# Kernel tuning notes

Hardware: AMD Instinct MI355X
Metric: run time of the kernel (lower is better)

Reference implementation:

```python
import jax, jax.numpy as jnp
import numpy as np

B, S, DM, H, NM, PRED = 32, 512, 512, 8, 4, 96
DK = DM // H
C1 = (NM + 7) // 2  # 5
C2 = (NM + 7) // 4  # 2
FC_IN = C2 * (S // 2)  # 512
EPS_NORM = 1e-12
EPS_LN = 1e-5


def _pos_encoding(seq_len, d):
    pos = np.arange(seq_len, dtype=np.float32)[:, None]
    div = np.exp(np.arange(0, d, 2, dtype=np.float32) * (-np.log(10000.0) / d))
    pe = np.zeros((seq_len, d), np.float32)
    pe[:, 0::2] = np.sin(pos * div)
    pe[:, 1::2] = np.cos(pos * div)
    return jnp.asarray(pe)

PE = _pos_encoding(S, DM)


def setup_inputs() -> dict:
    key = jax.random.key(0)
    ks = jax.random.split(key, 24)
    g = lambda k, shape, s: (jax.random.normal(k, shape, dtype=jnp.float32) * s)
    inp = {
        "x": g(ks[0], (B, S, 7), 1.0),
        "emb_W": g(ks[1], (4, DM), 0.5),
        "emb_b": jnp.zeros((DM,), jnp.float32),
        "Wq": g(ks[2], (NM, DM, DM), DM ** -0.5),
        "bq": jnp.zeros((NM, DM), jnp.float32),
        "Wk": g(ks[3], (NM, DM, DM), DM ** -0.5),
        "bk": jnp.zeros((NM, DM), jnp.float32),
        "Wv": g(ks[4], (NM, DM, DM), DM ** -0.5),
        "bv": jnp.zeros((NM, DM), jnp.float32),
        "Wo": g(ks[5], (NM, DM, DM), DM ** -0.5),
        "bo": jnp.zeros((NM, DM), jnp.float32),
        "conv1_w": g(ks[6], (C1, NM * DM, 3), (NM * DM * 3) ** -0.5),
        "conv1_b": jnp.zeros((C1,), jnp.float32),
        "conv2_w": g(ks[7], (C2, C1, 3), (C1 * 3) ** -0.5),
        "conv2_b": jnp.zeros((C2,), jnp.float32),
        "fc1_w": g(ks[8], (FC_IN, 256), FC_IN ** -0.5),
        "fc1_b": jnp.zeros((256,), jnp.float32),
        "fc2_w": g(ks[9], (256, 128), 256 ** -0.5),
        "fc2_b": jnp.zeros((128,), jnp.float32),
        "fc3_w": g(ks[10], (128, PRED), 128 ** -0.5),
        "fc3_b": jnp.zeros((PRED,), jnp.float32),
        "ln_g": jnp.ones((PRED,), jnp.float32),
        "ln_b": jnp.zeros((PRED,), jnp.float32),
    }
    return inp


def _l2norm(v):
    n = jnp.linalg.norm(v, axis=-1, keepdims=True)
    return v / jnp.maximum(n, EPS_NORM)


def reference(x, emb_W, emb_b, Wq, bq, Wk, bk, Wv, bv, Wo, bo,
              conv1_w, conv1_b, conv2_w, conv2_b,
              fc1_w, fc1_b, fc2_w, fc2_b, fc3_w, fc3_b, ln_g, ln_b):
    b, s, _ = x.shape
    static = x[:, :, :3]                     # [B,S,3]
    dynamic = x[:, :, 3:]                    # [B,S,4]
    # per-modality input: [dynamic_i | static] -> [B,M,S,4]
    mod_in = jnp.concatenate([
        dynamic.transpose(0, 2, 1)[..., None],
        jnp.broadcast_to(static[:, None], (b, NM, s, 3)),
    ], axis=-1)
    h = jnp.einsum('bmsf,fd->bmsd', mod_in, emb_W) + emb_b  # shared embedding
    h = h + PE[None, None, :s, :]

    # per-modality multi-head cosine attention (stacked over modality axis m)
    def proj(W, bias):
        y = jnp.einsum('bmsd,mde->bmse', h, W) + bias[None, :, None, :]
        return y.reshape(b, NM, s, H, DK).transpose(0, 1, 3, 2, 4)  # [B,M,H,S,DK]

    Q = _l2norm(proj(Wq, bq))
    K = _l2norm(proj(Wk, bk))
    V = proj(Wv, bv)
    scores = jnp.einsum('bmhsk,bmhtk->bmhst', Q, K)
    attn = jax.nn.softmax(scores, axis=-1)
    ctx = jnp.einsum('bmhst,bmhtk->bmhsk', attn, V)
    ctx = ctx.transpose(0, 1, 3, 2, 4).reshape(b, NM, s, DM)
    out = jnp.einsum('bmsd,mde->bmse', ctx, Wo) + bo[None, :, None, :]

    # concat modalities along feature dim: [B,S,M*DM]
    combined = out.transpose(0, 2, 1, 3).reshape(b, s, NM * DM)

    # conv stack (NCW layout), kernel 3, padding 1
    c = combined.transpose(0, 2, 1)  # [B, M*DM, S]
    dn = ('NCH', 'OIH', 'NCH')
    c = jax.lax.conv_general_dilated(c, conv1_w, (1,), ((1, 1),), dimension_numbers=dn) + conv1_b[None, :, None]
    c = jax.nn.elu(c)
    c = jax.lax.conv_general_dilated(c, conv2_w, (1,), ((1, 1),), dimension_numbers=dn) + conv2_b[None, :, None]
    c = jax.nn.elu(c)
    # max pool k=2 stride=2
    c = c.reshape(b, C2, s // 2, 2).max(axis=-1)
    flat = c.reshape(b, -1)  # [B, FC_IN]

    z = jax.nn.elu(flat @ fc1_w + fc1_b)
    z = jax.nn.elu(z @ fc2_w + fc2_b)
    z = z @ fc3_w + fc3_b  # [B, PRED]

    mu = jnp.mean(z, axis=-1, keepdims=True)
    var = jnp.var(z, axis=-1, keepdims=True)
    z = (z - mu) / jnp.sqrt(var + EPS_LN) * ln_g + ln_b
    return z.reshape(b, PRED, 1)
```

## Files before the change

### kernel.cpp

```cpp
#include <hip/hip_runtime.h>
#include <math.h>

typedef unsigned short u16;
typedef unsigned int u32;
typedef __attribute__((ext_vector_type(8))) short short8;
typedef __attribute__((ext_vector_type(4))) float f32x4;
typedef __attribute__((ext_vector_type(16))) float f32x16;
typedef __attribute__((ext_vector_type(4))) u32 u32x4;
typedef __attribute__((ext_vector_type(2))) u32 u32x2;

__device__ inline u16 f2b(float f) {
  u32 u = __builtin_bit_cast(u32, f);
  u32 r = u + 0x7fffu + ((u >> 16) & 1u);
  return (u16)(r >> 16);
}
__device__ inline float b2f(u16 b) {
  return __builtin_bit_cast(float, (u32)b << 16);
}
__device__ inline u32 cvtpk(float lo, float hi) {
  u32 r;
  asm("v_cvt_pk_bf16_f32 %0, %1, %2" : "=v"(r) : "v"(lo), "v"(hi));
  return r;
}
__device__ inline float eluf(float x) { return x > 0.f ? x : expf(x) - 1.f; }

__device__ inline f32x4 mfma16(short8 a, short8 b, f32x4 c) {
  return __builtin_amdgcn_mfma_f32_16x16x32_bf16(a, b, c, 0, 0, 0);
}
__device__ inline f32x16 mfma32(short8 a, short8 b, f32x16 c) {
  return __builtin_amdgcn_mfma_f32_32x32x16_bf16(a, b, c, 0, 0, 0);
}
__device__ inline void gload16(const u16* g, u16* l) {
  __builtin_amdgcn_global_load_lds((__attribute__((address_space(1))) void*)(g),
                                   (__attribute__((address_space(3))) void*)(l),
                                   16, 0, 0);
}

__global__ __launch_bounds__(256) void prep_misc(
    const float* __restrict__ emb_b, const float* __restrict__ bq,
    const float* __restrict__ bk, const float* __restrict__ bv,
    const float* __restrict__ Wq, const float* __restrict__ Wk,
    const float* __restrict__ Wv, const float* __restrict__ embW,
    const float* __restrict__ Wo, const float* __restrict__ bo,
    const float* __restrict__ w1, u16* __restrict__ A_pe,
    float* __restrict__ pb_bias, float* __restrict__ EW,
    u16* __restrict__ WEFFT, float* __restrict__ bias_t,
    u16* __restrict__ WTqkv) {
  __shared__ float smem[64 * 65];
  const int bid = blockIdx.x, t = threadIdx.x;
  if (bid < 512) {
    int s = bid;
    float div = __expf((2.f * t) * (-9.210340371976184f / 512.f));
    float arg = (float)s * div;
    A_pe[s * 512 + 2 * t] = f2b(__sinf(arg) + emb_b[2 * t]);
    A_pe[s * 512 + 2 * t + 1] = f2b(__cosf(arg) + emb_b[2 * t + 1]);
  } else if (bid < 536) {
    int i = (bid - 512) * 256 + t;
    int z = i >> 9, e = i & 511;
    int ty = z >> 2, m = z & 3;
    const float* bp = (ty == 0) ? bq : (ty == 1) ? bk : bv;
    pb_bias[i] = bp[m * 512 + e];
  } else if (bid < 584) {
    int idx = bid - 536;
    int z = idx >> 2, ch = idx & 3;
    const float* W =
        ((z < 4) ? Wq : (z < 8) ? Wk : Wv) + (long)(z & 3) * 262144;
    int el = t & 127, dh = t >> 7;
    int e = ch * 128 + el;
    float a[4] = {};
    for (int d = dh * 256; d < dh * 256 + 256; ++d) {
      float wv = W[(long)d * 512 + e];
#pragma unroll
      for (int f = 0; f < 4; ++f) a[f] += embW[f * 512 + d] * wv;
    }
#pragma unroll
    for (int f = 0; f < 4; ++f) smem[(dh * 4 + f) * 128 + el] = a[f];
    __syncthreads();
    if (t < 128) {
#pragma unroll
      for (int f = 0; f < 4; ++f)
        EW[((long)z * 4 + f) * 512 + e] =
            smem[f * 128 + el] + smem[(4 + f) * 128 + el];
    }
  } else if (bid < 1097) {
    const int wb = bid - 584;
    const int w = t >> 6, l = t & 63;
    if (wb < 512) {
      int idx = wb * 4 + w;
      int m = idx >> 9, d = idx & 511;
      const float* wrow = Wo + ((long)m * 512 + d) * 512;
      float a[15] = {};
#pragma unroll
      for (int i = 0; i < 8; ++i) {
        int e = l * 8 + i;
        float wv = wrow[e];
#pragma unroll
        for (int o = 0; o < 5; ++o)
#pragma unroll
          for (int k = 0; k < 3; ++k)
            a[o * 3 + k] += wv * w1[((long)o * 2048 + m * 512 + e) * 3 + k];
      }
#pragma unroll
      for (int j = 0; j < 15; ++j) {
        float v = a[j];
        for (int o = 1; o < 64; o <<= 1) v += __shfl_xor(v, o);
        if (l == 0) WEFFT[((long)m * 16 + j) * 512 + d] = f2b(v);
      }
      if (l == 0) WEFFT[((long)m * 16 + 15) * 512 + d] = 0;
    } else if (w == 0) {
      float a[15] = {};
      for (int c = l; c < 2048; c += 64) {
        float bv = bo[c];
#pragma unroll
        for (int o = 0; o < 5; ++o)
#pragma unroll
          for (int k = 0; k < 3; ++k)
            a[o * 3 + k] += bv * w1[((long)o * 2048 + c) * 3 + k];
      }
#pragma unroll
      for (int j = 0; j < 15; ++j) {
        float v = a[j];
        for (int o = 1; o < 64; o <<= 1) v += __shfl_xor(v, o);
        if (l == 0) bias_t[j] = v;
      }
      if (l == 0) bias_t[15] = 0.f;
    }
  } else {
    int bidt = bid - 1097;
    int mid = bidt >> 6, rest = bidt & 63;
    int d0 = (rest >> 3) * 64, e0 = (rest & 7) * 64;
    const float* W =
        ((mid < 4) ? Wq : (mid < 8) ? Wk : Wv) + (long)(mid & 3) * 262144;
    u16* WT = WTqkv + (long)mid * 262144;
    float(*tile)[65] = (float(*)[65])smem;
    int dr = t >> 2, ec = (t & 3) * 16;
#pragma unroll
    for (int j = 0; j < 16; j += 4) {
      float4 v = *(const float4*)&W[(long)(d0 + dr) * 512 + e0 + ec + j];
      tile[dr][ec + j] = v.x;
      tile[dr][ec + j + 1] = v.y;
      tile[dr][ec + j + 2] = v.z;
      tile[dr][ec + j + 3] = v.w;
    }
    __syncthreads();
    int er = t >> 2, dc = (t & 3) * 16;
    u16 tmp[16] __attribute__((aligned(16)));
#pragma unroll
    for (int j = 0; j < 16; ++j) tmp[j] = f2b(tile[dc + j][er]);
    *(short8*)&WT[(long)(e0 + er) * 512 + d0 + dc] = *(short8*)&tmp[0];
    *(short8*)&WT[(long)(e0 + er) * 512 + d0 + dc + 8] = *(short8*)&tmp[8];
  }
}

template <bool OBF>
__global__ __launch_bounds__(256) void gemm_bt(
    const u16* __restrict__ A, long sAz, int lda, const u16* __restrict__ BT,
    const float* __restrict__ bias, void* __restrict__ out, long sOz, int ldo) {
  __shared__ u16 As[3][128 * 32];
  __shared__ u16 Bs[3][128 * 32];
  const int z = blockIdx.z;
  const int tid = threadIdx.x, w = tid >> 6, l = tid & 63;
  const long row0 = (long)blockIdx.y * 128;
  const u16* Ab = A + (long)z * sAz + row0 * lda;
  const u16* Bb = BT + (long)z * 262144 + (long)blockIdx.x * 128 * 512;
  const u16* ga = Ab + (long)(w * 32 + (l >> 2)) * lda + (l & 3) * 8;
  const u16* gb = Bb + (long)(w * 32 + (l >> 2)) * 512 + (l & 3) * 8;
  f32x4 acc[4][4] = {};
  const int wr = (w >> 1) * 64, wc = (w & 1) * 64;

#define GSTAGE(BF, KT)                                                        \
  {                                                                           \
    gload16(ga + (KT)*32, &As[BF][w * 32 * 32]);                              \
    gload16(ga + (KT)*32 + 16 * lda, &As[BF][w * 32 * 32 + 16 * 32]);         \
    gload16(gb + (KT)*32, &Bs[BF][w * 32 * 32]);                              \
    gload16(gb + (KT)*32 + 16 * 512, &Bs[BF][w * 32 * 32 + 16 * 32]);         \
  }

#define GTILE(KT, CUR, NXT)                                                   \
  {                                                                           \
    if ((KT) < 15) {                                                          \
      GSTAGE(NXT, (KT) + 1);                                                  \
      asm volatile("s_waitcnt vmcnt(4)" ::: "memory");                        \
    } else {                                                                  \
      asm volatile("s_waitcnt vmcnt(0)" ::: "memory");                        \
    }                                                                         \
    __builtin_amdgcn_s_barrier();                                             \
    __builtin_amdgcn_sched_barrier(0);                                        \
    short8 af[4], bf[4];                                                      \
    _Pragma("unroll") for (int i = 0; i < 4; ++i) af[i] =                     \
        *(const short8*)&As[CUR][(wr + i * 16 + (l & 15)) * 32 +              \
                                 (l >> 4) * 8];                               \
    _Pragma("unroll") for (int i = 0; i < 4; ++i) bf[i] =                     \
        *(const short8*)&Bs[CUR][(wc + i * 16 + (l & 15)) * 32 +              \
                                 (l >> 4) * 8];                               \
    _Pragma("unroll") for (int i = 0; i < 4; ++i) _Pragma("unroll")           \
        for (int j = 0; j < 4; ++j) acc[i][j] =                               \
            mfma16(af[i], bf[j], acc[i][j]);                                  \
    __builtin_amdgcn_sched_barrier(0);                                        \
  }

  GSTAGE(0, 0);
  GTILE(0, 0, 1);  GTILE(1, 1, 2);  GTILE(2, 2, 0);  GTILE(3, 0, 1);
  GTILE(4, 1, 2);  GTILE(5, 2, 0);  GTILE(6, 0, 1);  GTILE(7, 1, 2);
  GTILE(8, 2, 0);  GTILE(9, 0, 1);  GTILE(10, 1, 2); GTILE(11, 2, 0);
  GTILE(12, 0, 1); GTILE(13, 1, 2); GTILE(14, 2, 0); GTILE(15, 0, 1);
#undef GTILE
#undef GSTAGE

  const int colB = blockIdx.x * 128 + wc;
#pragma unroll
  for (int i = 0; i < 4; ++i)
#pragma unroll
    for (int j = 0; j < 4; ++j) {
      int col = colB + j * 16 + (l & 15);
      float bb = bias[(long)z * 512 + col];
#pragma unroll
      for (int q = 0; q < 4; ++q) {
        long r = row0 + wr + i * 16 + (l >> 4) * 4 + q;
        float v = acc[i][j][q] + bb;
        if (OBF)
          ((u16*)out)[(long)z * sOz + r * ldo + col] = f2b(v);
        else
          ((float*)out)[(long)z * sOz + r * ldo + col] = v;
      }
    }
}

__global__ __launch_bounds__(256) void kv_fused(
    const float* __restrict__ x, const float* __restrict__ EW,
    const u16* __restrict__ PB, u16* __restrict__ K, u16* __restrict__ VT,
    long mstride) {
  __shared__ float ews[2][4][64];
  __shared__ u16 vtile[64][72];
  const int bh = blockIdx.x;
  const int st = blockIdx.y;
  const int m = blockIdx.z;
  const int b = bh >> 3, h = bh & 7;
  const int hoff = h * 64;
  const int t = threadIdx.x;
  if (t < 128) {
    int ir = t >> 6, dk = t & 63;
    int z = (ir + 1) * 4 + m;
#pragma unroll
    for (int f = 0; f < 4; ++f)
      ews[ir][f][dk] = EW[((long)z * 4 + f) * 512 + hoff + dk];
  }
  __syncthreads();
  const int sr = t >> 2, cq = t & 3;
  const int s = st * 64 + sr;
  const long rid = (long)b * 512 + s;
  const float* xr = x + rid * 7;
  const float xd = xr[3 + m], x0 = xr[0], x1 = xr[1], x2 = xr[2];
  const long obase = (long)m * mstride + rid * 512 + hoff + cq * 16;

  float res[2][16];
#pragma unroll
  for (int ir = 0; ir < 2; ++ir) {
    int z = (ir + 1) * 4 + m;
    const u16* pbp = PB + (((long)z * 512 + s)) * 512 + hoff + cq * 16;
    short8 pbv0 = *(const short8*)pbp;
    short8 pbv1 = *(const short8*)(pbp + 8);
#pragma unroll
    for (int j = 0; j < 16; ++j) {
      int dk = cq * 16 + j;
      u16 pb = (u16)(j < 8 ? pbv0[j] : pbv1[j - 8]);
      res[ir][j] = xd * ews[ir][0][dk] + x0 * ews[ir][1][dk] +
                   x1 * ews[ir][2][dk] + x2 * ews[ir][3][dk] + b2f(pb);
    }
  }
  {
    float ss = 0.f;
#pragma unroll
    for (int j = 0; j < 16; ++j) ss += res[0][j] * res[0][j];
    ss += __shfl_xor(ss, 1);
    ss += __shfl_xor(ss, 2);
    float sc = 1.f / fmaxf(sqrtf(ss), 1e-12f);
    u32 o[8];
#pragma unroll
    for (int jj = 0; jj < 8; ++jj)
      o[jj] = cvtpk(res[0][2 * jj] * sc, res[0][2 * jj + 1] * sc);
    *(u32x4*)&K[obase] = *(u32x4*)&o[0];
    *(u32x4*)&K[obase + 8] = *(u32x4*)&o[4];
  }
  {
    u32 o[8];
#pragma unroll
    for (int jj = 0; jj < 8; ++jj)
      o[jj] = cvtpk(res[1][2 * jj], res[1][2 * jj + 1]);
    *(short8*)&vtile[sr][cq * 16] = *(short8*)&o[0];
    *(short8*)&vtile[sr][cq * 16 + 8] = *(short8*)&o[4];
  }
  __syncthreads();
  {
    int kr = t >> 2, sc2 = (t & 3) * 16;
    u16 tmp[16] __attribute__((aligned(16)));
#pragma unroll
    for (int j = 0; j < 16; ++j) tmp[j] = vtile[sc2 + j][kr];
    long gdst = (long)m * mstride + ((long)bh * 64 + kr) * 512 + st * 64 + sc2;
    *(short8*)&VT[gdst] = *(short8*)&tmp[0];
    *(short8*)&VT[gdst + 8] = *(short8*)&tmp[8];
  }
}

__global__ __launch_bounds__(512, 2) void attn_kernel(
    const float* __restrict__ x, const float* __restrict__ EW,
    const u16* __restrict__ PB, const u16* __restrict__ Kg,
    const u16* __restrict__ VTg, u16* __restrict__ ctxg, long mstride) {
  __shared__ u16 Kb[4][64][64];
  __shared__ u16 Vb[4][64][64];
  __shared__ float ewsq[4][64];
  const int wgid = (blockIdx.x & 7) * 256 + (blockIdx.x >> 3);
  const int qp = wgid & 1;
  const int mz = wgid >> 1;
  const int m = mz & 3;
  const int bh = mz >> 2;
  const u16* K = Kg + (long)m * mstride;
  const u16* VT = VTg + (long)m * mstride;
  u16* ctx = ctxg + (long)m * mstride;
  const int b = bh >> 3, h = bh & 7;
  const int tid = threadIdx.x, w = tid >> 6, l = tid & 63;
  const int lq = l & 31, hi = l >> 5, l7 = l & 7;
  const long rowbase = (long)b * 512;
  const int hoff = h * 64;
  const int rw = l >> 3, gch = (l & 7) ^ rw;
  const int qrow = qp * 256 + w * 32;

  if (tid < 256) {
    int f = tid >> 6, dk = tid & 63;
    ewsq[f][dk] = EW[((long)m * 4 + f) * 512 + hoff + dk];
  }
  __syncthreads();

  short8 qf[4];
  {
    const int s_q = qrow + lq;
    const float* xr = x + (rowbase + s_q) * 7;
    const float xd = xr[3 + m], x0 = xr[0], x1 = xr[1], x2 = xr[2];
    float qv[4][8];
    float ss = 0.f;
#pragma unroll
    for (int dc = 0; dc < 4; ++dc) {
      const int dk0 = dc * 16 + hi * 8;
      const u16* pbq = PB + ((long)m * 512 + s_q) * 512 + hoff + dk0;
      short8 pbv = *(const short8*)pbq;
#pragma unroll
      for (int j = 0; j < 8; ++j) {
        int dk = dk0 + j;
        float v = xd * ewsq[0][dk] + x0 * ewsq[1][dk] + x1 * ewsq[2][dk] +
                  x2 * ewsq[3][dk] + b2f((u16)pbv[j]);
        qv[dc][j] = v;
        ss += v * v;
      }
    }
    ss += __shfl_xor(ss, 32);
    float sc = 1.f / fmaxf(sqrtf(ss), 1e-12f);
#pragma unroll
    for (int dc = 0; dc < 4; ++dc) {
      u32x4 pk = {cvtpk(qv[dc][0] * sc, qv[dc][1] * sc),
                  cvtpk(qv[dc][2] * sc, qv[dc][3] * sc),
                  cvtpk(qv[dc][4] * sc, qv[dc][5] * sc),
                  cvtpk(qv[dc][6] * sc, qv[dc][7] * sc)};
      qf[dc] = __builtin_bit_cast(short8, pk);
    }
  }

  short8 ones;
#pragma unroll
  for (int i = 0; i < 8; ++i) ones[i] = (short)0x3F80;

  f32x16 o_acc[2] = {};
  f32x16 l_acc = {};

  const u16* Kgbase = K + rowbase * 512 + hoff + gch * 8;
  const u16* Vgbase = VT + (long)bh * 64 * 512 + gch * 8;

#define STAGE(bf, kt)                                                         \
  {                                                                           \
    int rr = w * 8;                                                           \
    gload16(Kgbase + (long)((kt)*64 + rr + rw) * 512, &Kb[bf][rr][0]);        \
    gload16(Vgbase + (long)(rr + rw) * 512 + (kt)*64, &Vb[bf][rr][0]);        \
  }

#define TILE(KT, CUR, NXT)                                                    \
  {                                                                           \
    if ((KT) < 6) {                                                           \
      STAGE(NXT, (KT) + 2);                                                   \
      asm volatile("s_waitcnt vmcnt(4)" ::: "memory");                        \
    } else if ((KT) == 6) {                                                   \
      asm volatile("s_waitcnt vmcnt(2)" ::: "memory");                        \
    } else {                                                                  \
      asm volatile("s_waitcnt vmcnt(0)" ::: "memory");                        \
    }                                                                         \
    __builtin_amdgcn_s_barrier();                                             \
    __builtin_amdgcn_sched_barrier(0);                                        \
    __builtin_amdgcn_s_setprio(1);                                            \
    _Pragma("unroll") for (int ktile = 0; ktile < 2; ++ktile) {               \
      f32x16 s = {};                                                          \
      _Pragma("unroll") for (int dc = 0; dc < 4; ++dc) {                      \
        short8 kf = *(const short8*)((const char*)&Kb[CUR][ktile * 32 + lq]   \
                                         [0] +                                \
                                     (((dc * 2 + hi) ^ l7) * 16));            \
        s = mfma32(kf, qf[dc], s);                                            \
      }                                                                       \
      float p[16];                                                            \
      _Pragma("unroll") for (int r = 0; r < 16; ++r) p[r] = __expf(s[r]);     \
      u32 s0a = cvtpk(p[0], p[1]), s0b = cvtpk(p[4], p[5]);                   \
      u32 s1a = cvtpk(p[2], p[3]), s1b = cvtpk(p[6], p[7]);                   \
      u32 s2a = cvtpk(p[8], p[9]), s2b = cvtpk(p[12], p[13]);                 \
      u32 s3a = cvtpk(p[10], p[11]), s3b = cvtpk(p[14], p[15]);               \
      asm("v_permlane32_swap_b32 %0, %1" : "+v"(s0a), "+v"(s0b));             \
      asm("v_permlane32_swap_b32 %0, %1" : "+v"(s1a), "+v"(s1b));             \
      asm("v_permlane32_swap_b32 %0, %1" : "+v"(s2a), "+v"(s2b));             \
      asm("v_permlane32_swap_b32 %0, %1" : "+v"(s3a), "+v"(s3b));             \
      u32x4 f0v = {s0a, s1a, s0b, s1b};                                       \
      u32x4 f1v = {s2a, s3a, s2b, s3b};                                       \
      short8 bf0 = __builtin_bit_cast(short8, f0v);                           \
      short8 bf1 = __builtin_bit_cast(short8, f1v);                           \
      _Pragma("unroll") for (int kk2 = 0; kk2 < 2; ++kk2) {                   \
        const int kc = ktile * 2 + kk2;                                       \
        short8 pb = kk2 ? bf1 : bf0;                                          \
        l_acc = mfma32(ones, pb, l_acc);                                      \
        _Pragma("unroll") for (int dt = 0; dt < 2; ++dt) {                    \
          short8 vf =                                                         \
              *(const short8*)((const char*)&Vb[CUR][dt * 32 + lq][0] +       \
                               (((kc * 2 + hi) ^ l7) * 16));                  \
          o_acc[dt] = mfma32(vf, pb, o_acc[dt]);                              \
        }                                                                     \
      }                                                                       \
    }                                                                         \
    __builtin_amdgcn_s_setprio(0);                                            \
    __builtin_amdgcn_sched_barrier(0);                                        \
  }

  STAGE(0, 0);
  STAGE(1, 1);
  TILE(0, 0, 2);
  TILE(1, 1, 3);
  TILE(2, 2, 0);
  TILE(3, 3, 1);
  TILE(4, 0, 2);
  TILE(5, 1, 3);
  TILE(6, 2, 0);
  TILE(7, 3, 1);
#undef TILE
#undef STAGE
  const float inv = 1.f / l_acc[0];
  u16* crow = ctx + (rowbase + qrow + lq) * 512 + hoff + hi * 4;
#pragma unroll
  for (int dt = 0; dt < 2; ++dt)
#pragma unroll
    for (int rq = 0; rq < 4; ++rq) {
      u32 w0 = cvtpk(o_acc[dt][rq * 4 + 0] * inv, o_acc[dt][rq * 4 + 1] * inv);
      u32 w1 = cvtpk(o_acc[dt][rq * 4 + 2] * inv, o_acc[dt][rq * 4 + 3] * inv);
      u32x2 pr = {w0, w1};
      *(u32x2*)&crow[dt * 32 + rq * 8] = pr;
    }
}

__global__ __launch_bounds__(64) void t_gemm(const u16* __restrict__ ctx4,
                                             const u16* __restrict__ WEFFT,
                                             float* __restrict__ t) {
  const int l = threadIdx.x;
  const long r0 = (long)blockIdx.x * 16;
  f32x4 acc = {};
#pragma unroll
  for (int m = 0; m < 4; ++m) {
    const u16* A =
        ctx4 + (long)m * 8388608 + (r0 + (l & 15)) * 512 + (l >> 4) * 8;
    const u16* Bb = WEFFT + m * 8192 + (l & 15) * 512 + (l >> 4) * 8;
#pragma unroll
    for (int kt = 0; kt < 16; ++kt) {
      short8 af = *(const short8*)(A + kt * 32);
      short8 bf = *(const short8*)(Bb + kt * 32);
      acc = mfma16(af, bf, acc);
    }
  }
#pragma unroll
  for (int q = 0; q < 4; ++q)
    t[(r0 + (l >> 4) * 4 + q) * 16 + (l & 15)] = acc[q];
}

__global__ __launch_bounds__(512) void tail_fused(
    const float* __restrict__ t, const float* __restrict__ bias_t,
    const float* __restrict__ b1, const float* __restrict__ w2,
    const float* __restrict__ b2, const float* __restrict__ fw1,
    const float* __restrict__ fb1, const float* __restrict__ fw2,
    const float* __restrict__ fb2, const float* __restrict__ fw3,
    const float* __restrict__ fb3, const float* __restrict__ g,
    const float* __restrict__ be, float* __restrict__ out) {
  __shared__ float ts[512][16];
  __shared__ float c1s[5][512];
  __shared__ float flat[512];
  __shared__ float z1p[2][256];
  __shared__ float z1[256];
  __shared__ float z2p[2][128];
  __shared__ float z2[128];
  __shared__ float z3[96];
  int b = blockIdx.x, tid = threadIdx.x;
  const float4* tsrc = (const float4*)(t + (long)b * 8192);
  float4* tdst = (float4*)&ts[0][0];
#pragma unroll
  for (int i = 0; i < 4; ++i) tdst[tid + i * 512] = tsrc[tid + i * 512];
  __syncthreads();
#pragma unroll
  for (int i = 0; i < 5; ++i) {
    int idx = tid + i * 512;
    int o = idx >> 9, s = idx & 511;
    float a = b1[o];
#pragma unroll
    for (int k = 0; k < 3; ++k) {
      int ss = s + k - 1;
      if (ss >= 0 && ss < 512) a += ts[ss][o * 3 + k] + bias_t[o * 3 + k];
    }
    c1s[o][s] = eluf(a);
  }
  __syncthreads();
  {
    int r = tid;
    int o = r >> 8, sp = r & 255;
    float mx = -1e30f;
#pragma unroll
    for (int sd = 0; sd < 2; ++sd) {
      int s = sp * 2 + sd;
      float a = b2[o];
#pragma unroll
      for (int ic = 0; ic < 5; ++ic)
#pragma unroll
        for (int k = 0; k < 3; ++k) {
          int ss = s + k - 1;
          if (ss >= 0 && ss < 512) a += c1s[ic][ss] * w2[(o * 5 + ic) * 3 + k];
        }
      mx = fmaxf(mx, eluf(a));
    }
    flat[r] = mx;
  }
  __syncthreads();
  {
    int o = tid & 255, part = tid >> 8;
    float a = 0.f;
    const float* wp = fw1 + (long)part * 256 * 256 + o;
    const float* xp = flat + part * 256;
#pragma unroll 8
    for (int i = 0; i < 256; ++i) a += xp[i] * wp[i * 256];
    z1p[part][o] = a;
  }
  __syncthreads();
  if (tid < 256) z1[tid] = eluf(fb1[tid] + z1p[0][tid] + z1p[1][tid]);
  __syncthreads();
  if (tid < 256) {
    int o = tid & 127, part = tid >> 7;
    float a = 0.f;
    const float* wp = fw2 + (long)part * 128 * 128 + o;
    const float* xp = z1 + part * 128;
#pragma unroll 8
    for (int i = 0; i < 128; ++i) a += xp[i] * wp[i * 128];
    z2p[part][o] = a;
  }
  __syncthreads();
  if (tid < 128) z2[tid] = eluf(fb2[tid] + z2p[0][tid] + z2p[1][tid]);
  __syncthreads();
  if (tid < 96) {
    float a = fb3[tid];
#pragma unroll 8
    for (int i = 0; i < 128; ++i) a += z2[i] * fw3[i * 96 + tid];
    z3[tid] = a;
  }
  __syncthreads();
  if (tid < 96) {
    float mu = 0.f;
    for (int j = 0; j < 96; ++j) mu += z3[j];
    mu *= (1.f / 96.f);
    float sq = 0.f;
    for (int j = 0; j < 96; ++j) {
      float d = z3[j] - mu;
      sq += d * d;
    }
    float var = sq * (1.f / 96.f);
    out[b * 96 + tid] = (z3[tid] - mu) / sqrtf(var + 1e-5f) * g[tid] + be[tid];
  }
}

extern "C" void kernel_launch(void* const* d_in, const int* in_sizes, int n_in,
                              void* d_out, int out_size, void* d_ws,
                              size_t ws_size, hipStream_t stream) {
  (void)in_sizes; (void)n_in; (void)out_size;
  const float* x    = (const float*)d_in[0];
  const float* embW = (const float*)d_in[1];
  const float* embB = (const float*)d_in[2];
  const float* Wq   = (const float*)d_in[3];
  const float* bq   = (const float*)d_in[4];
  const float* Wk   = (const float*)d_in[5];
  const float* bk   = (const float*)d_in[6];
  const float* Wv   = (const float*)d_in[7];
  const float* bv   = (const float*)d_in[8];
  const float* Wo   = (const float*)d_in[9];
  const float* bo   = (const float*)d_in[10];
  const float* c1w  = (const float*)d_in[11];
  const float* c1b  = (const float*)d_in[12];
  const float* c2w  = (const float*)d_in[13];
  const float* c2b  = (const float*)d_in[14];
  const float* f1w  = (const float*)d_in[15];
  const float* f1b  = (const float*)d_in[16];
  const float* f2w  = (const float*)d_in[17];
  const float* f2b_ = (const float*)d_in[18];
  const float* f3w  = (const float*)d_in[19];
  const float* f3b  = (const float*)d_in[20];
  const float* lng  = (const float*)d_in[21];
  const float* lnb  = (const float*)d_in[22];
  float* out = (float*)d_out;

  char* p = (char*)d_ws;
  const size_t NEED = 215736384;
  if (ws_size < NEED) return;
  const long MS = 8388608;

  u16*   A_pe    = (u16*)(p + 0);
  u16*   WTqkv   = (u16*)(p + 524288);
  float* pb_bias = (float*)(p + 6815744);
  float* EW      = (float*)(p + 6840320);
  u16*   PB      = (u16*)(p + 6938624);
  u16*   ctx4    = (u16*)(p + 13230080);
  u16*   K4      = (u16*)(p + 80338944);
  u16*   VT4     = (u16*)(p + 147447808);
  u16*   WEFFT   = (u16*)(p + 214556672);
  float* bias_t  = (float*)(p + 214622208);
  float* t_buf   = (float*)(p + 214622272);

  prep_misc<<<1865, 256, 0, stream>>>(embB, bq, bk, bv, Wq, Wk, Wv, embW, Wo,
                                      bo, c1w, A_pe, pb_bias, EW, WEFFT,
                                      bias_t, WTqkv);
  gemm_bt<true><<<dim3(4, 4, 12), 256, 0, stream>>>(
      A_pe, 0, 512, WTqkv, pb_bias, (void*)PB, 262144, 512);

  kv_fused<<<dim3(256, 8, 4), 256, 0, stream>>>(x, EW, PB, K4, VT4, MS);
  attn_kernel<<<2048, 512, 0, stream>>>(x, EW, PB, K4, VT4, ctx4, MS);

  t_gemm<<<1024, 64, 0, stream>>>(ctx4, WEFFT, t_buf);
  tail_fused<<<32, 512, 0, stream>>>(t_buf, bias_t, c1b, c2w, c2b, f1w, f1b,
                                     f2w, f2b_, f3w, f3b, lng, lnb, out);
}
```

Before: 222.5 us.

## Shrink attention LDS ring to three buffers and raise occupancy to four blocks

```diff
diff --git a/kernel.cpp b/kernel.cpp
--- a/kernel.cpp
+++ b/kernel.cpp
@@ -302,12 +302,12 @@
   }
 }
 
-__global__ __launch_bounds__(512, 2) void attn_kernel(
+__global__ __launch_bounds__(512, 4) void attn_kernel(
     const float* __restrict__ x, const float* __restrict__ EW,
     const u16* __restrict__ PB, const u16* __restrict__ Kg,
     const u16* __restrict__ VTg, u16* __restrict__ ctxg, long mstride) {
-  __shared__ u16 Kb[4][64][64];
-  __shared__ u16 Vb[4][64][64];
+  __shared__ u16 Kb[3][64][64];
+  __shared__ u16 Vb[3][64][64];
   __shared__ float ewsq[4][64];
   const int wgid = (blockIdx.x & 7) * 256 + (blockIdx.x >> 3);
   const int qp = wgid & 1;
@@ -325,41 +325,56 @@
   const int rw = l >> 3, gch = (l & 7) ^ rw;
   const int qrow = qp * 256 + w * 32;
 
+  const u16* Kgbase = K + rowbase * 512 + hoff + gch * 8;
+  const u16* Vgbase = VT + (long)bh * 64 * 512 + gch * 8;
+
+#define STAGE(bf, kt)                                                         \
+  {                                                                           \
+    int rr = w * 8;                                                           \
+    gload16(Kgbase + (long)((kt)*64 + rr + rw) * 512, &Kb[bf][rr][0]);        \
+    gload16(Vgbase + (long)(rr + rw) * 512 + (kt)*64, &Vb[bf][rr][0]);        \
+  }
+
   if (tid < 256) {
     int f = tid >> 6, dk = tid & 63;
     ewsq[f][dk] = EW[((long)m * 4 + f) * 512 + hoff + dk];
   }
   __syncthreads();
+  STAGE(0, 0);
 
   short8 qf[4];
   {
     const int s_q = qrow + lq;
     const float* xr = x + (rowbase + s_q) * 7;
     const float xd = xr[3 + m], x0 = xr[0], x1 = xr[1], x2 = xr[2];
-    float qv[4][8];
+    const u16* pbq = PB + ((long)m * 512 + s_q) * 512 + hoff + hi * 8;
+    u32 qpk[16];
     float ss = 0.f;
 #pragma unroll
     for (int dc = 0; dc < 4; ++dc) {
-      const int dk0 = dc * 16 + hi * 8;
-      const u16* pbq = PB + ((long)m * 512 + s_q) * 512 + hoff + dk0;
-      short8 pbv = *(const short8*)pbq;
+      short8 pbv = *(const short8*)(pbq + dc * 16);
+      float v[8];
 #pragma unroll
       for (int j = 0; j < 8; ++j) {
-        int dk = dk0 + j;
-        float v = xd * ewsq[0][dk] + x0 * ewsq[1][dk] + x1 * ewsq[2][dk] +
-                  x2 * ewsq[3][dk] + b2f((u16)pbv[j]);
-        qv[dc][j] = v;
-        ss += v * v;
+        int dk = dc * 16 + hi * 8 + j;
+        v[j] = xd * ewsq[0][dk] + x0 * ewsq[1][dk] + x1 * ewsq[2][dk] +
+               x2 * ewsq[3][dk] + b2f((u16)pbv[j]);
+        ss += v[j] * v[j];
       }
+#pragma unroll
+      for (int jj = 0; jj < 4; ++jj)
+        qpk[dc * 4 + jj] = cvtpk(v[2 * jj], v[2 * jj + 1]);
     }
     ss += __shfl_xor(ss, 32);
     float sc = 1.f / fmaxf(sqrtf(ss), 1e-12f);
 #pragma unroll
     for (int dc = 0; dc < 4; ++dc) {
-      u32x4 pk = {cvtpk(qv[dc][0] * sc, qv[dc][1] * sc),
-                  cvtpk(qv[dc][2] * sc, qv[dc][3] * sc),
-                  cvtpk(qv[dc][4] * sc, qv[dc][5] * sc),
-                  cvtpk(qv[dc][6] * sc, qv[dc][7] * sc)};
+      u32x4 pk;
+#pragma unroll
+      for (int jj = 0; jj < 4; ++jj) {
+        u32 pv = qpk[dc * 4 + jj];
+        pk[jj] = cvtpk(b2f((u16)pv) * sc, b2f((u16)(pv >> 16)) * sc);
+      }
       qf[dc] = __builtin_bit_cast(short8, pk);
     }
   }
@@ -371,22 +386,10 @@
   f32x16 o_acc[2] = {};
   f32x16 l_acc = {};
 
-  const u16* Kgbase = K + rowbase * 512 + hoff + gch * 8;
-  const u16* Vgbase = VT + (long)bh * 64 * 512 + gch * 8;
-
-#define STAGE(bf, kt)                                                         \
-  {                                                                           \
-    int rr = w * 8;                                                           \
-    gload16(Kgbase + (long)((kt)*64 + rr + rw) * 512, &Kb[bf][rr][0]);        \
-    gload16(Vgbase + (long)(rr + rw) * 512 + (kt)*64, &Vb[bf][rr][0]);        \
-  }
-
 #define TILE(KT, CUR, NXT)                                                    \
   {                                                                           \
-    if ((KT) < 6) {                                                           \
-      STAGE(NXT, (KT) + 2);                                                   \
-      asm volatile("s_waitcnt vmcnt(4)" ::: "memory");                        \
-    } else if ((KT) == 6) {                                                   \
+    if ((KT) < 7) {                                                           \
+      STAGE(NXT, (KT) + 1);                                                   \
       asm volatile("s_waitcnt vmcnt(2)" ::: "memory");                        \
     } else {                                                                  \
       asm volatile("s_waitcnt vmcnt(0)" ::: "memory");                        \
@@ -432,16 +435,14 @@
     __builtin_amdgcn_sched_barrier(0);                                        \
   }
 
-  STAGE(0, 0);
-  STAGE(1, 1);
-  TILE(0, 0, 2);
-  TILE(1, 1, 3);
+  TILE(0, 0, 1);
+  TILE(1, 1, 2);
   TILE(2, 2, 0);
-  TILE(3, 3, 1);
-  TILE(4, 0, 2);
-  TILE(5, 1, 3);
-  TILE(6, 2, 0);
-  TILE(7, 3, 1);
+  TILE(3, 0, 1);
+  TILE(4, 1, 2);
+  TILE(5, 2, 0);
+  TILE(6, 0, 1);
+  TILE(7, 1, 2);
 #undef TILE
 #undef STAGE
   const float inv = 1.f / l_acc[0];
```

Measured after the change: 208.2 us. 1.07x faster.
